# Kernel tuning notes

Measured on AMD Instinct MI355X. Metric: run time of the kernel, lower is better.

Reference implementation:

```python
import jax, jax.numpy as jnp
import numpy as np

N, E, HID, H, L, EF = 50000, 640000, 128, 8, 3, 16
C = HID // H  # 16, per-head output channels (concat=True)
NEG_SLOPE = 0.2
LN_EPS = 1e-5


def setup_inputs() -> dict:
    key = jax.random.key(0)
    ks = jax.random.split(key, 12)
    s = 0.05
    x = jax.random.normal(ks[0], (N, HID), jnp.float32)
    batch_index = jnp.sort(jax.random.randint(ks[1], (N,), 0, 64, dtype=jnp.int32))
    edge_index = jax.random.randint(ks[2], (2, E), 0, N, dtype=jnp.int32)
    edge_attr = jax.random.normal(ks[3], (E, EF), jnp.float32)
    # edge_transform: Linear(EF, HID)
    Wt = jax.random.normal(ks[4], (EF, HID), jnp.float32) * s
    bt = jnp.zeros((HID,), jnp.float32)
    # per-layer GATv2 params (stacked over L layers)
    Wl = jax.random.normal(ks[5], (L, HID, HID), jnp.float32) * s  # lin_l (source)
    bl = jnp.zeros((L, HID), jnp.float32)
    Wr = jax.random.normal(ks[6], (L, HID, HID), jnp.float32) * s  # lin_r (target)
    br = jnp.zeros((L, HID), jnp.float32)
    We = jax.random.normal(ks[7], (L, HID, HID), jnp.float32) * s  # lin_edge (no bias)
    att = jax.random.normal(ks[8], (L, H, C), jnp.float32) * s
    bias_o = jnp.zeros((L, HID), jnp.float32)
    ln_g = jnp.ones((L, HID), jnp.float32)
    ln_b = jnp.zeros((L, HID), jnp.float32)
    return dict(x=x, batch_index=batch_index, edge_index=edge_index, edge_attr=edge_attr,
                Wt=Wt, bt=bt, Wl=Wl, bl=bl, Wr=Wr, br=br, We=We, att=att,
                bias_o=bias_o, ln_g=ln_g, ln_b=ln_b)


def _layer_norm(x, g, b):
    mu = jnp.mean(x, axis=-1, keepdims=True)
    var = jnp.var(x, axis=-1, keepdims=True)
    return g * (x - mu) * jax.lax.rsqrt(var + LN_EPS) + b


def _gatv2_layer(x, ea, src, dst, Wl, bl, Wr, br, We, att, bias_o):
    # node transforms: lin_l for source features, lin_r for target features
    xl = (x @ Wl + bl).reshape(N, H, C)
    xr = (x @ Wr + br).reshape(N, H, C)
    em = (ea @ We).reshape(E, H, C)
    # per-edge attention logits (GATv2: leaky_relu AFTER the sum, then dot with att)
    m = jax.nn.leaky_relu(xl[src] + xr[dst] + em, NEG_SLOPE)  # [E,H,C]
    logits = jnp.einsum('ehc,hc->eh', m, att)                  # [E,H]
    # segment softmax over incoming edges of each destination node
    lmax = jax.ops.segment_max(logits, dst, num_segments=N)    # [N,H]
    p = jnp.exp(logits - lmax[dst])
    denom = jax.ops.segment_sum(p, dst, num_segments=N)        # [N,H]
    alpha = p / (denom[dst] + 1e-16)
    # weighted scatter-aggregate of source messages
    out = jax.ops.segment_sum(xl[src] * alpha[:, :, None], dst, num_segments=N)  # [N,H,C]
    return out.reshape(N, HID) + bias_o


def reference(x, batch_index, edge_index, edge_attr, Wt, bt, Wl, bl, Wr, br, We, att, bias_o, ln_g, ln_b):
    src, dst = edge_index[0], edge_index[1]
    ea = edge_attr @ Wt + bt  # shared edge_transform, [E,HID]
    for l in range(L):
        out = _gatv2_layer(x, ea, src, dst, Wl[l], bl[l], Wr[l], br[l], We[l], att[l], bias_o[l])
        out = _layer_norm(out, ln_g[l], ln_b[l])
        x = jax.nn.relu(out) + x  # dropout p=0 -> identity; residual
    return x
```

## Files before the change

### kernel.cpp

```cpp
#include <hip/hip_runtime.h>

#define N_NODES 50000
#define N_EDGES 640000
#define HID 128
#define EF 16
#define NLAYERS 3
#define CHUNK 32
#define SCAN_BLOCKS 196

typedef __attribute__((ext_vector_type(8))) short short8;
typedef __attribute__((ext_vector_type(4))) float f32x4;
typedef __attribute__((ext_vector_type(2))) float f32x2;

__device__ __forceinline__ unsigned short f2bf(float f) {
  unsigned int u = __float_as_uint(f);
  u = u + 0x7FFFu + ((u >> 16) & 1u);
  return (unsigned short)(u >> 16);
}

__device__ __forceinline__ float dpp_hadd8(float v) {
  int x;
  x = __builtin_amdgcn_update_dpp(0, __float_as_int(v), 0xB1, 0xF, 0xF, true);
  v += __int_as_float(x);
  x = __builtin_amdgcn_update_dpp(0, __float_as_int(v), 0x4E, 0xF, 0xF, true);
  v += __int_as_float(x);
  x = __builtin_amdgcn_update_dpp(0, __float_as_int(v), 0x141, 0xF, 0xF, true);
  v += __int_as_float(x);
  return v;
}

__device__ __forceinline__ f32x2 pk_fma_lo(f32x2 d, f32x2 v, f32x2 pair) {
  asm("v_pk_fma_f32 %0, %1, %2, %0 op_sel_hi:[1,0,1]"
      : "+v"(d) : "v"(v), "v"(pair));
  return d;
}
__device__ __forceinline__ f32x2 pk_fma_hi(f32x2 d, f32x2 v, f32x2 pair) {
  asm("v_pk_fma_f32 %0, %1, %2, %0 op_sel:[0,1,0] op_sel_hi:[1,1,1]"
      : "+v"(d) : "v"(v), "v"(pair));
  return d;
}
__device__ __forceinline__ f32x2 pk_add(f32x2 a, f32x2 b) {
  f32x2 d;
  asm("v_pk_add_f32 %0, %1, %2" : "=v"(d) : "v"(a), "v"(b));
  return d;
}
__device__ __forceinline__ f32x2 pk_mul(f32x2 a, f32x2 b) {
  f32x2 d;
  asm("v_pk_mul_f32 %0, %1, %2" : "=v"(d) : "v"(a), "v"(b));
  return d;
}

__device__ __forceinline__ int pslot(int j) {
  return (((j >> 4) * 8 + (j & 7)) << 1) + ((j >> 3) & 1);
}

__global__ __launch_bounds__(256) void k_setup(const float* __restrict__ Wt,
                                               const float* __restrict__ bt,
                                               const float* __restrict__ We,
                                               const float* __restrict__ Wl,
                                               const float* __restrict__ Wr,
                                               const float* __restrict__ x,
                                               float* __restrict__ Mt,
                                               float* __restrict__ ct,
                                               unsigned short* __restrict__ WT,
                                               unsigned short* __restrict__ xbf) {
  int b = blockIdx.x, t = threadIdx.x;
  if (b < 26) {
    int id = b * 256 + t;
    const int total = NLAYERS * (EF + 1) * HID;
    if (id >= total) return;
    int l = id / ((EF + 1) * HID);
    int r = id % ((EF + 1) * HID);
    int row = r / HID;
    int j = r % HID;
    const float* Wel = We + l * HID * HID;
    float s = 0.f;
    if (row < EF) {
      const float* wtr = Wt + row * HID;
      for (int i = 0; i < HID; ++i) s += wtr[i] * Wel[i * HID + j];
      Mt[(l * EF + row) * HID + pslot(j)] = s;
    } else {
      for (int i = 0; i < HID; ++i) s += bt[i] * Wel[i * HID + j];
      ct[l * HID + pslot(j)] = s;
    }
  } else if (b < 410) {
    int id = (b - 26) * 256 + t;
    int k = id & (HID - 1);
    int n = (id >> 7) & (HID - 1);
    int s = (id >> 14) & 1;
    int l = id >> 15;
    const float* W = (s == 0 ? Wl : Wr) + (size_t)l * HID * HID;
    WT[id] = f2bf(W[k * HID + n]);
  } else {
    int id = (b - 410) * 256 + t;
    const float4* p = (const float4*)(x + (size_t)id * 8);
    float4 a = p[0], bb = p[1];
    unsigned short o[8] = {f2bf(a.x), f2bf(a.y), f2bf(a.z), f2bf(a.w),
                           f2bf(bb.x), f2bf(bb.y), f2bf(bb.z), f2bf(bb.w)};
    *(uint4*)(xbf + (size_t)id * 8) = *(uint4*)o;
  }
}

__global__ __launch_bounds__(256) void k_hist(const int* __restrict__ dst, int* __restrict__ counts) {
  int e = blockIdx.x * 256 + threadIdx.x;
  if (e < N_EDGES) atomicAdd(&counts[dst[e]], 1);
}

__global__ __launch_bounds__(256) void k_scan1(const int* __restrict__ counts,
                                               int* __restrict__ rowptr,
                                               int* __restrict__ bsum) {
  __shared__ int sc[256];
  int t = threadIdx.x;
  int i = blockIdx.x * 256 + t;
  int v = (i < N_NODES) ? counts[i] : 0;
  sc[t] = v;
  __syncthreads();
  for (int off = 1; off < 256; off <<= 1) {
    int u = 0;
    if (t >= off) u = sc[t - off];
    __syncthreads();
    sc[t] += u;
    __syncthreads();
  }
  if (i < N_NODES) rowptr[i] = sc[t] - v;
  if (t == 255) bsum[blockIdx.x] = sc[255];
}

__global__ __launch_bounds__(256) void k_scan2(int* __restrict__ bsum) {
  __shared__ int sc[256];
  int t = threadIdx.x;
  int v = (t < SCAN_BLOCKS) ? bsum[t] : 0;
  sc[t] = v;
  __syncthreads();
  for (int off = 1; off < 256; off <<= 1) {
    int u = 0;
    if (t >= off) u = sc[t - off];
    __syncthreads();
    sc[t] += u;
    __syncthreads();
  }
  bsum[t] = sc[t] - v;
}

__global__ __launch_bounds__(256) void k_scan3(int* __restrict__ rowptr, const int* __restrict__ bsum) {
  int t = threadIdx.x;
  int i = blockIdx.x * 256 + t;
  if (i < N_NODES) rowptr[i] += bsum[blockIdx.x];
  if (i == 0) rowptr[N_NODES] = N_EDGES;
}

__global__ __launch_bounds__(256) void k_fill(const int* __restrict__ src,
                                              const int* __restrict__ dst,
                                              const int* __restrict__ rowptr,
                                              int* __restrict__ fill,
                                              int* __restrict__ ssrc,
                                              const float* __restrict__ eattr,
                                              float* __restrict__ easrt) {
  int e = blockIdx.x * 256 + threadIdx.x;
  if (e >= N_EDGES) return;
  int d = dst[e];
  int pos = atomicAdd(&fill[d], 1);
  int idx = rowptr[d] + pos;
  ssrc[idx] = src[e] << 6;
  const float4* pe = (const float4*)(eattr + (size_t)e * EF);
  float4* po = (float4*)(easrt + (size_t)idx * EF);
#pragma unroll
  for (int q = 0; q < 4; ++q) po[q] = pe[q];
}

__global__ __launch_bounds__(256) void k_gemm_mfma(const unsigned short* __restrict__ xbf,
                                                   const unsigned short* __restrict__ WTl,
                                                   const float* __restrict__ bl,
                                                   const float* __restrict__ br,
                                                   const float* __restrict__ ctl,
                                                   unsigned short* __restrict__ xlb,
                                                   unsigned short* __restrict__ xrb) {
  __shared__ short As[64 * 136];
  __shared__ short Bs[128 * 136];
  int t = threadIdx.x;
  int s = blockIdx.y;
  int row0 = blockIdx.x * 64;

  const uint4* gx = (const uint4*)xbf;
#pragma unroll
  for (int p = 0; p < 4; ++p) {
    int c = t + p * 256;
    int row = c >> 4, col16 = c & 15;
    int grow = row0 + row;
    if (grow >= N_NODES) grow = N_NODES - 1;
    uint4 v = gx[grow * 16 + col16];
    *(uint4*)(&As[row * 136 + col16 * 8]) = v;
  }
  const uint4* gw = (const uint4*)WTl;
#pragma unroll
  for (int p = 0; p < 8; ++p) {
    int c = t + p * 256;
    int row = c >> 4, col16 = c & 15;
    uint4 v = gw[s * 2048 + row * 16 + col16];
    *(uint4*)(&Bs[row * 136 + col16 * 8]) = v;
  }
  __syncthreads();

  int lane = t & 63, w = t >> 6;
  int quad = lane >> 4, lm = lane & 15;
  f32x4 acc[4][2];
#pragma unroll
  for (int mf = 0; mf < 4; ++mf)
#pragma unroll
    for (int nf = 0; nf < 2; ++nf) acc[mf][nf] = (f32x4)(0.f);

#pragma unroll
  for (int ks = 0; ks < 4; ++ks) {
    short8 af[4], bf[2];
#pragma unroll
    for (int mf = 0; mf < 4; ++mf)
      af[mf] = *(short8*)(&As[(mf * 16 + lm) * 136 + ks * 32 + quad * 8]);
#pragma unroll
    for (int nf = 0; nf < 2; ++nf)
      bf[nf] = *(short8*)(&Bs[(w * 32 + nf * 16 + lm) * 136 + ks * 32 + quad * 8]);
#pragma unroll
    for (int mf = 0; mf < 4; ++mf)
#pragma unroll
      for (int nf = 0; nf < 2; ++nf)
        acc[mf][nf] = __builtin_amdgcn_mfma_f32_16x16x32_bf16(af[mf], bf[nf], acc[mf][nf], 0, 0, 0);
  }

  const float* bias = (s == 0) ? bl : br;
  unsigned short* out = (s == 0) ? xlb : xrb;
#pragma unroll
  for (int nf = 0; nf < 2; ++nf) {
    int n = w * 32 + nf * 16 + lm;
    int slot = pslot(n);
    float bv = bias[n] + ((s == 1) ? ctl[slot] : 0.f);
#pragma unroll
    for (int mf = 0; mf < 4; ++mf) {
#pragma unroll
      for (int r = 0; r < 4; ++r) {
        int grow = row0 + mf * 16 + quad * 4 + r;
        if (grow < N_NODES) out[(size_t)grow * HID + slot] = f2bf(acc[mf][nf][r] + bv);
      }
    }
  }
}

__global__ __launch_bounds__(64) void k_fused(const float* __restrict__ xin,
                                              const unsigned int* __restrict__ xlb,
                                              const unsigned int* __restrict__ xrb,
                                              const int* __restrict__ rowptr,
                                              const int* __restrict__ ssrc,
                                              const float* __restrict__ easrt,
                                              const float* __restrict__ Mt,
                                              const float* __restrict__ att,
                                              const float* __restrict__ bias_o,
                                              const float* __restrict__ lng,
                                              const float* __restrict__ lnb,
                                              float* __restrict__ xout,
                                              unsigned short* __restrict__ xbf_out) {
  __shared__ __align__(16) float ea_s[CHUNK][EF];
  __shared__ int src_s[CHUNK + 8];
  int n = blockIdx.x;
  int l = threadIdx.x;
  int j0 = (l >> 3) * 16 + (l & 7), j1 = j0 + 8;

  f32x2 mtp[EF];
#pragma unroll
  for (int k = 0; k < EF; ++k) mtp[k] = *(const f32x2*)(&Mt[k * HID + l * 2]);
  unsigned int ur = xrb[(size_t)n * 64 + l];
  f32x2 base;
  base.x = __uint_as_float(ur << 16);
  base.y = __uint_as_float(ur & 0xFFFF0000u);
  const float LOG2E = 1.44269504088896340736f;
  f32x2 attp = {att[j0] * LOG2E, att[j1] * LOG2E};
  f32x2 c02 = {0.2f, 0.2f};
  int beg = rowptr[n], end = rowptr[n + 1];

  f32x2 acc = {0.f, 0.f};
  float denom = 0.f;

  for (int c0 = beg; c0 < end; c0 += CHUNK) {
    int cnt = min(CHUNK, end - c0);
    if (l < cnt) src_s[l] = ssrc[c0 + l];
    if (l < 8) src_s[cnt + l] = 0;
    for (int q = l; q < cnt * 4; q += 64) {
      int i = q >> 2, part = q & 3;
      *(float4*)(&ea_s[i][part * 4]) =
          *(const float4*)(easrt + (size_t)(c0 + i) * EF + part * 4);
    }

    auto edge = [&](int i, unsigned int u) {
      f32x2 xls;
      xls.x = __uint_as_float(u << 16);
      xls.y = __uint_as_float(u & 0xFFFF0000u);
      f32x2 m = pk_add(base, xls);
      const f32x4* er = (const f32x4*)(&ea_s[i][0]);
      f32x4 e0 = er[0], e1 = er[1], e2 = er[2], e3 = er[3];
      f32x2 p01 = __builtin_shufflevector(e0, e0, 0, 1);
      f32x2 p23 = __builtin_shufflevector(e0, e0, 2, 3);
      f32x2 p45 = __builtin_shufflevector(e1, e1, 0, 1);
      f32x2 p67 = __builtin_shufflevector(e1, e1, 2, 3);
      f32x2 p89 = __builtin_shufflevector(e2, e2, 0, 1);
      f32x2 pAB = __builtin_shufflevector(e2, e2, 2, 3);
      f32x2 pCD = __builtin_shufflevector(e3, e3, 0, 1);
      f32x2 pEF = __builtin_shufflevector(e3, e3, 2, 3);
      m = pk_fma_lo(m, mtp[0], p01);
      m = pk_fma_hi(m, mtp[1], p01);
      m = pk_fma_lo(m, mtp[2], p23);
      m = pk_fma_hi(m, mtp[3], p23);
      m = pk_fma_lo(m, mtp[4], p45);
      m = pk_fma_hi(m, mtp[5], p45);
      m = pk_fma_lo(m, mtp[6], p67);
      m = pk_fma_hi(m, mtp[7], p67);
      m = pk_fma_lo(m, mtp[8], p89);
      m = pk_fma_hi(m, mtp[9], p89);
      m = pk_fma_lo(m, mtp[10], pAB);
      m = pk_fma_hi(m, mtp[11], pAB);
      m = pk_fma_lo(m, mtp[12], pCD);
      m = pk_fma_hi(m, mtp[13], pCD);
      m = pk_fma_lo(m, mtp[14], pEF);
      m = pk_fma_hi(m, mtp[15], pEF);
      f32x2 ms = pk_mul(c02, m);
      m.x = fmaxf(m.x, ms.x);
      m.y = fmaxf(m.y, ms.y);
      f32x2 v2 = pk_mul(m, attp);
      float vs = dpp_hadd8(v2.x + v2.y);
      float p = exp2f(vs);
      denom += p;
      acc.x = fmaf(xls.x, p, acc.x);
      acc.y = fmaf(xls.y, p, acc.y);
    };

    unsigned int cur[4];
#pragma unroll
    for (int q = 0; q < 4; ++q) cur[q] = xlb[src_s[q] + l];
    int cnt4 = cnt & ~3;
    for (int i = 0; i < cnt4; i += 4) {
      unsigned int nxt[4];
#pragma unroll
      for (int q = 0; q < 4; ++q) nxt[q] = xlb[src_s[i + 4 + q] + l];
#pragma unroll
      for (int q = 0; q < 4; ++q) edge(i + q, cur[q]);
#pragma unroll
      for (int q = 0; q < 4; ++q) cur[q] = nxt[q];
    }
#pragma unroll
    for (int q = 0; q < 4; ++q)
      if (cnt4 + q < cnt) edge(cnt4 + q, cur[q]);
  }

  f32x2 outp;
  float inv = 1.f / (denom + 1e-16f);
  outp.x = acc.x * inv + bias_o[j0];
  outp.y = acc.y * inv + bias_o[j1];
  float s1 = outp.x + outp.y;
  float s2 = outp.x * outp.x + outp.y * outp.y;
#pragma unroll
  for (int mask = 1; mask <= 32; mask <<= 1) {
    s1 += __shfl_xor(s1, mask);
    s2 += __shfl_xor(s2, mask);
  }
  float mu = s1 * (1.f / 128.f);
  float var = s2 * (1.f / 128.f) - mu * mu;
  float rs = rsqrtf(var + 1e-5f);
  float y0 = lng[j0] * (outp.x - mu) * rs + lnb[j0];
  float y1 = lng[j1] * (outp.y - mu) * rs + lnb[j1];
  float r0 = fmaxf(y0, 0.f) + xin[(size_t)n * HID + j0];
  float r1 = fmaxf(y1, 0.f) + xin[(size_t)n * HID + j1];
  xout[(size_t)n * HID + j0] = r0;
  xout[(size_t)n * HID + j1] = r1;
  xbf_out[(size_t)n * HID + j0] = f2bf(r0);
  xbf_out[(size_t)n * HID + j1] = f2bf(r1);
}

extern "C" void kernel_launch(void* const* d_in, const int* in_sizes, int n_in,
                              void* d_out, int out_size, void* d_ws, size_t ws_size,
                              hipStream_t stream) {
  const float* x0    = (const float*)d_in[0];
  const int*   eidx  = (const int*)d_in[2];
  const float* eattr = (const float*)d_in[3];
  const float* Wt    = (const float*)d_in[4];
  const float* bt    = (const float*)d_in[5];
  const float* Wl    = (const float*)d_in[6];
  const float* bl    = (const float*)d_in[7];
  const float* Wr    = (const float*)d_in[8];
  const float* br    = (const float*)d_in[9];
  const float* We    = (const float*)d_in[10];
  const float* att   = (const float*)d_in[11];
  const float* bo    = (const float*)d_in[12];
  const float* lng   = (const float*)d_in[13];
  const float* lnb   = (const float*)d_in[14];
  float* out = (float*)d_out;
  const int* src = eidx;
  const int* dst = eidx + N_EDGES;

  char* ws = (char*)d_ws;
  size_t off = 0;
  auto alloc = [&](size_t bytes) {
    char* p = ws + off;
    off += (bytes + 255) & ~(size_t)255;
    return p;
  };
  int* counts = (int*)alloc((size_t)N_NODES * 4);
  int* fill   = (int*)alloc((size_t)N_NODES * 4);
  float* Mt   = (float*)alloc((size_t)NLAYERS * EF * HID * 4);
  float* ct   = (float*)alloc((size_t)NLAYERS * HID * 4);
  int* rowptr = (int*)alloc((size_t)(N_NODES + 1) * 4);
  int* bsum   = (int*)alloc(256 * 4);
  int* ssrc   = (int*)alloc((size_t)N_EDGES * 4);
  float* easrt = (float*)alloc((size_t)N_EDGES * EF * 4);
  unsigned short* xlb = (unsigned short*)alloc((size_t)N_NODES * HID * 2);
  unsigned short* xrb = (unsigned short*)alloc((size_t)N_NODES * HID * 2);
  float* xbuf = (float*)alloc((size_t)N_NODES * HID * 4);
  unsigned short* xbf = (unsigned short*)alloc((size_t)N_NODES * HID * 2);
  unsigned short* WTb = (unsigned short*)alloc((size_t)NLAYERS * 2 * HID * HID * 2);

  hipMemsetAsync(counts, 0, (char*)(fill + N_NODES) - (char*)counts, stream);

  hipLaunchKernelGGL(k_setup, dim3(3535), dim3(256), 0, stream,
                     Wt, bt, We, Wl, Wr, x0, Mt, ct, WTb, xbf);
  hipLaunchKernelGGL(k_hist, dim3((N_EDGES + 255) / 256), dim3(256), 0, stream, dst, counts);
  hipLaunchKernelGGL(k_scan1, dim3(SCAN_BLOCKS), dim3(256), 0, stream, counts, rowptr, bsum);
  hipLaunchKernelGGL(k_scan2, dim3(1), dim3(256), 0, stream, bsum);
  hipLaunchKernelGGL(k_scan3, dim3(SCAN_BLOCKS), dim3(256), 0, stream, rowptr, bsum);
  hipLaunchKernelGGL(k_fill, dim3((N_EDGES + 255) / 256), dim3(256), 0, stream,
                     src, dst, rowptr, fill, ssrc, eattr, easrt);

  for (int l = 0; l < NLAYERS; ++l) {
    const float* xin = (l == 0) ? x0 : (const float*)xbuf;
    float* xout = (l == NLAYERS - 1) ? out : xbuf;
    hipLaunchKernelGGL(k_gemm_mfma, dim3((N_NODES + 63) / 64, 2), dim3(256), 0, stream,
                       xbf, WTb + (size_t)l * 2 * HID * HID, bl + l * HID, br + l * HID,
                       ct + (size_t)l * HID, xlb, xrb);
    hipLaunchKernelGGL(k_fused, dim3(N_NODES), dim3(64), 0, stream,
                       xin, (const unsigned int*)xlb, (const unsigned int*)xrb,
                       rowptr, ssrc, easrt,
                       Mt + (size_t)l * EF * HID, att + l * HID,
                       bo + l * HID, lng + l * HID, lnb + l * HID, xout, xbf);
  }
}
```

Measured before the change: 486.5 us.

## Sort nodes by in-degree and pack four node-wavefronts per fused block

```diff
diff --git a/kernel.cpp b/kernel.cpp
--- a/kernel.cpp
+++ b/kernel.cpp
@@ -7,6 +7,7 @@
 #define NLAYERS 3
 #define CHUNK 32
 #define SCAN_BLOCKS 196
+#define FUSED_WPB 4
 
 typedef __attribute__((ext_vector_type(8))) short short8;
 typedef __attribute__((ext_vector_type(4))) float f32x4;
@@ -106,6 +107,47 @@
   if (e < N_EDGES) atomicAdd(&counts[dst[e]], 1);
 }
 
+__global__ __launch_bounds__(256) void k_dhist(const int* __restrict__ counts,
+                                               int* __restrict__ dcnt) {
+  __shared__ int h[64];
+  int t = threadIdx.x;
+  if (t < 64) h[t] = 0;
+  __syncthreads();
+  int i = blockIdx.x * 256 + t;
+  if (i < N_NODES) {
+    int d = counts[i];
+    int b = 63 - min(d, 63);
+    atomicAdd(&h[b], 1);
+  }
+  __syncthreads();
+  if (t < 64 && h[t]) atomicAdd(&dcnt[t], h[t]);
+}
+
+__global__ __launch_bounds__(64) void k_dscan(const int* __restrict__ dcnt,
+                                              int* __restrict__ dstart) {
+  int t = threadIdx.x;
+  int v = dcnt[t];
+  int x = v;
+#pragma unroll
+  for (int off = 1; off < 64; off <<= 1) {
+    int u = __shfl_up(x, off);
+    if (t >= off) x += u;
+  }
+  dstart[t] = x - v;
+}
+
+__global__ __launch_bounds__(256) void k_dfill(const int* __restrict__ counts,
+                                               const int* __restrict__ dstart,
+                                               int* __restrict__ dfill,
+                                               int* __restrict__ perm) {
+  int i = blockIdx.x * 256 + threadIdx.x;
+  if (i >= N_NODES) return;
+  int d = counts[i];
+  int b = 63 - min(d, 63);
+  int pos = atomicAdd(&dfill[b], 1);
+  perm[dstart[b] + pos] = i;
+}
+
 __global__ __launch_bounds__(256) void k_scan1(const int* __restrict__ counts,
                                                int* __restrict__ rowptr,
                                                int* __restrict__ bsum) {
@@ -243,23 +285,28 @@
   }
 }
 
-__global__ __launch_bounds__(64) void k_fused(const float* __restrict__ xin,
-                                              const unsigned int* __restrict__ xlb,
-                                              const unsigned int* __restrict__ xrb,
-                                              const int* __restrict__ rowptr,
-                                              const int* __restrict__ ssrc,
-                                              const float* __restrict__ easrt,
-                                              const float* __restrict__ Mt,
-                                              const float* __restrict__ att,
-                                              const float* __restrict__ bias_o,
-                                              const float* __restrict__ lng,
-                                              const float* __restrict__ lnb,
-                                              float* __restrict__ xout,
-                                              unsigned short* __restrict__ xbf_out) {
-  __shared__ __align__(16) float ea_s[CHUNK][EF];
-  __shared__ int src_s[CHUNK + 8];
-  int n = blockIdx.x;
-  int l = threadIdx.x;
+__global__ __launch_bounds__(64 * FUSED_WPB) void k_fused(
+    const float* __restrict__ xin,
+    const unsigned int* __restrict__ xlb,
+    const unsigned int* __restrict__ xrb,
+    const int* __restrict__ rowptr,
+    const int* __restrict__ ssrc,
+    const float* __restrict__ easrt,
+    const float* __restrict__ Mt,
+    const float* __restrict__ att,
+    const float* __restrict__ bias_o,
+    const float* __restrict__ lng,
+    const float* __restrict__ lnb,
+    const int* __restrict__ perm,
+    float* __restrict__ xout,
+    unsigned short* __restrict__ xbf_out) {
+  __shared__ __align__(16) float ea_all[FUSED_WPB][CHUNK][EF];
+  __shared__ int src_all[FUSED_WPB][CHUNK + 8];
+  int w = threadIdx.x >> 6;
+  int l = threadIdx.x & 63;
+  int n = perm[blockIdx.x * FUSED_WPB + w];
+  float(*ea_s)[EF] = ea_all[w];
+  int* src_s = src_all[w];
   int j0 = (l >> 3) * 16 + (l & 7), j1 = j0 + 8;
 
   f32x2 mtp[EF];
@@ -401,10 +448,14 @@
   };
   int* counts = (int*)alloc((size_t)N_NODES * 4);
   int* fill   = (int*)alloc((size_t)N_NODES * 4);
+  int* dcnt   = (int*)alloc(64 * 4);
+  int* dfill  = (int*)alloc(64 * 4);
   float* Mt   = (float*)alloc((size_t)NLAYERS * EF * HID * 4);
   float* ct   = (float*)alloc((size_t)NLAYERS * HID * 4);
   int* rowptr = (int*)alloc((size_t)(N_NODES + 1) * 4);
   int* bsum   = (int*)alloc(256 * 4);
+  int* dstart = (int*)alloc(64 * 4);
+  int* perm   = (int*)alloc((size_t)N_NODES * 4);
   int* ssrc   = (int*)alloc((size_t)N_EDGES * 4);
   float* easrt = (float*)alloc((size_t)N_EDGES * EF * 4);
   unsigned short* xlb = (unsigned short*)alloc((size_t)N_NODES * HID * 2);
@@ -413,11 +464,15 @@
   unsigned short* xbf = (unsigned short*)alloc((size_t)N_NODES * HID * 2);
   unsigned short* WTb = (unsigned short*)alloc((size_t)NLAYERS * 2 * HID * HID * 2);
 
-  hipMemsetAsync(counts, 0, (char*)(fill + N_NODES) - (char*)counts, stream);
+  hipMemsetAsync(counts, 0, (char*)(dfill + 64) - (char*)counts, stream);
 
   hipLaunchKernelGGL(k_setup, dim3(3535), dim3(256), 0, stream,
                      Wt, bt, We, Wl, Wr, x0, Mt, ct, WTb, xbf);
   hipLaunchKernelGGL(k_hist, dim3((N_EDGES + 255) / 256), dim3(256), 0, stream, dst, counts);
+  hipLaunchKernelGGL(k_dhist, dim3(SCAN_BLOCKS), dim3(256), 0, stream, counts, dcnt);
+  hipLaunchKernelGGL(k_dscan, dim3(1), dim3(64), 0, stream, dcnt, dstart);
+  hipLaunchKernelGGL(k_dfill, dim3(SCAN_BLOCKS), dim3(256), 0, stream,
+                     counts, dstart, dfill, perm);
   hipLaunchKernelGGL(k_scan1, dim3(SCAN_BLOCKS), dim3(256), 0, stream, counts, rowptr, bsum);
   hipLaunchKernelGGL(k_scan2, dim3(1), dim3(256), 0, stream, bsum);
   hipLaunchKernelGGL(k_scan3, dim3(SCAN_BLOCKS), dim3(256), 0, stream, rowptr, bsum);
@@ -430,10 +485,10 @@
     hipLaunchKernelGGL(k_gemm_mfma, dim3((N_NODES + 63) / 64, 2), dim3(256), 0, stream,
                        xbf, WTb + (size_t)l * 2 * HID * HID, bl + l * HID, br + l * HID,
                        ct + (size_t)l * HID, xlb, xrb);
-    hipLaunchKernelGGL(k_fused, dim3(N_NODES), dim3(64), 0, stream,
+    hipLaunchKernelGGL(k_fused, dim3(N_NODES / FUSED_WPB), dim3(64 * FUSED_WPB), 0, stream,
                        xin, (const unsigned int*)xlb, (const unsigned int*)xrb,
                        rowptr, ssrc, easrt,
                        Mt + (size_t)l * EF * HID, att + l * HID,
-                       bo + l * HID, lng + l * HID, lnb + l * HID, xout, xbf);
-  }
-}
+                       bo + l * HID, lng + l * HID, lnb + l * HID, perm, xout, xbf);
+  }
+}
```

Result: slower. 673.8 us (+38.5%).
